# Performance work log

Measured on AMD Instinct MI355X. Metric: run time of the kernel, lower is better.

The kernel has to match this reference:

```python
import jax, jax.numpy as jnp
import numpy as np

D_MODEL = 1024
N_HEAD = 16
D_K = D_MODEL // N_HEAD


def setup_inputs() -> dict:
    key = jax.random.key(0)
    ks = jax.random.split(key, 11)
    B, T = 2, 2048
    s = 1.0 / np.sqrt(D_MODEL)
    return {
        "q": jax.random.normal(ks[0], (B, T, D_MODEL), jnp.float32),
        "k": jax.random.normal(ks[1], (B, T, D_MODEL), jnp.float32),
        "v": jax.random.normal(ks[2], (B, T, D_MODEL), jnp.float32),
        "w_q": jax.random.normal(ks[3], (D_MODEL, D_MODEL), jnp.float32) * s,
        "b_q": jax.random.normal(ks[4], (D_MODEL,), jnp.float32) * 0.01,
        "w_k": jax.random.normal(ks[5], (D_MODEL, D_MODEL), jnp.float32) * s,
        "b_k": jax.random.normal(ks[6], (D_MODEL,), jnp.float32) * 0.01,
        "w_v": jax.random.normal(ks[7], (D_MODEL, D_MODEL), jnp.float32) * s,
        "b_v": jax.random.normal(ks[8], (D_MODEL,), jnp.float32) * 0.01,
        "w_o": jax.random.normal(ks[9], (D_MODEL, D_MODEL), jnp.float32) * s,
        "b_o": jax.random.normal(ks[10], (D_MODEL,), jnp.float32) * 0.01,
    }


def reference(q, k, v, w_q, b_q, w_k, b_k, w_v, b_v, w_o, b_o):
    B, T, _ = q.shape
    # QKV projections -> [B, H, T, d_k]
    def proj(x, w, b):
        return (jnp.einsum('btd,de->bte', x, w) + b).reshape(B, T, N_HEAD, D_K).transpose(0, 2, 1, 3)
    qh = proj(q, w_q, b_q)
    kh = proj(k, w_k, b_k)
    vh = proj(v, w_v, b_v)
    scale = jnp.float32(1.0 / np.sqrt(D_K))
    scores = jnp.einsum('bhqd,bhkd->bhqk', qh, kh) * scale  # [B,H,T,T]
    attn = jax.nn.softmax(scores, axis=-1)
    # dropout is identity in eval mode
    out = jnp.einsum('bhqk,bhkd->bhqd', attn, vh)  # [B,H,T,d_k]
    out = out.transpose(0, 2, 1, 3).reshape(B, T, N_HEAD * D_K)
    return jnp.einsum('btd,de->bte', out, w_o) + b_o
```

## Files before the change

### kernel.cpp

```cpp
#include <hip/hip_runtime.h>
#include <stdint.h>

#define DEVI static __device__ __forceinline__

typedef float f32x4 __attribute__((ext_vector_type(4)));
typedef float f32x16 __attribute__((ext_vector_type(16)));
typedef short s16x8 __attribute__((ext_vector_type(8)));
typedef unsigned short u16x4 __attribute__((ext_vector_type(4)));
typedef uint32_t u32x2 __attribute__((ext_vector_type(2)));
typedef uint32_t u32x4 __attribute__((ext_vector_type(4)));

DEVI unsigned short f2bf(float f) {
  union { float f; uint32_t u; } v; v.f = f;
  uint32_t u = v.u;
  return (unsigned short)((u + 0x7fffu + ((u >> 16) & 1u)) >> 16);
}

DEVI float bf2f(unsigned short u) {
  union { uint32_t u; float f; } v;
  v.u = ((uint32_t)u) << 16;
  return v.f;
}

DEVI uint32_t cvtpk(float lo, float hi) {
  uint32_t r;
  asm("v_cvt_pk_bf16_f32 %0, %1, %2" : "=v"(r) : "v"(lo), "v"(hi));
  return r;
}

DEVI float fexp2(float x) {
#if __has_builtin(__builtin_amdgcn_exp2f)
  return __builtin_amdgcn_exp2f(x);
#else
  return exp2f(x);
#endif
}

DEVI void pl32swap(uint32_t& a, uint32_t& b) {
#if __has_builtin(__builtin_amdgcn_permlane32_swap)
  u32x2 r = __builtin_amdgcn_permlane32_swap(a, b, false, false);
  a = r[0]; b = r[1];
#else
  asm("v_permlane32_swap_b32 %0, %1" : "+v"(a), "+v"(b));
#endif
}

DEVI float swap_half(float x, int hi) {
  uint32_t a = __float_as_uint(x), b = a;
  pl32swap(a, b);
  return hi ? __uint_as_float(a) : __uint_as_float(b);
}

DEVI void g2l16(const void* g, void* l) {
  __builtin_amdgcn_global_load_lds(
      (const __attribute__((address_space(1))) void*)g,
      (__attribute__((address_space(3))) void*)l, 16, 0, 0);
}

DEVI float vmax16(const f32x16& v) {
  float a = fmaxf(fmaxf(v[0], v[1]), fmaxf(v[2], v[3]));
  float b = fmaxf(fmaxf(v[4], v[5]), fmaxf(v[6], v[7]));
  float c = fmaxf(fmaxf(v[8], v[9]), fmaxf(v[10], v[11]));
  float d = fmaxf(fmaxf(v[12], v[13]), fmaxf(v[14], v[15]));
  return fmaxf(fmaxf(a, b), fmaxf(c, d));
}

DEVI float vsum16(const f32x16& v) {
  float a = (v[0] + v[1]) + (v[2] + v[3]);
  float b = (v[4] + v[5]) + (v[6] + v[7]);
  float c = (v[8] + v[9]) + (v[10] + v[11]);
  float d = (v[12] + v[13]) + (v[14] + v[15]);
  return (a + b) + (c + d);
}

__global__ __launch_bounds__(256) void k_cvt3(const float* __restrict__ q,
                                              const float* __restrict__ k,
                                              const float* __restrict__ v,
                                              unsigned short* __restrict__ out) {
  const int y = blockIdx.y;
  const float* in = y == 0 ? q : y == 1 ? k : v;
  unsigned short* o = out + (size_t)y * 4194304;
  int idx = blockIdx.x * blockDim.x + threadIdx.x;
  int stride = gridDim.x * blockDim.x;
  for (int i = idx * 4; i < 4194304; i += stride * 4) {
    f32x4 x = *(const f32x4*)(in + i);
    u16x4 r;
    for (int j = 0; j < 4; ++j) r[j] = f2bf(x[j]);
    *(u16x4*)(o + i) = r;
  }
}

__global__ __launch_bounds__(256) void k_wt4(const float* w0, const float* w1,
                                             const float* w2, const float* w3,
                                             unsigned short* t0, unsigned short* t1,
                                             unsigned short* t2, unsigned short* t3) {
  const int z = blockIdx.z;
  const float* w = z == 0 ? w0 : z == 1 ? w1 : z == 2 ? w2 : w3;
  unsigned short* wt = z == 0 ? t0 : z == 1 ? t1 : z == 2 ? t2 : t3;
  __shared__ float tile[32][33];
  const int tx = threadIdx.x, ty = threadIdx.y;
  const int n0 = blockIdx.x * 32, k0 = blockIdx.y * 32;
  for (int j = 0; j < 4; ++j)
    tile[ty + j * 8][tx] = w[(size_t)(k0 + ty + j * 8) * 1024 + n0 + tx];
  __syncthreads();
  for (int j = 0; j < 4; ++j)
    wt[(size_t)(n0 + ty + j * 8) * 1024 + k0 + tx] = f2bf(tile[tx][ty + j * 8]);
}

__global__ __launch_bounds__(256) void k_gemm_multi(
    const unsigned short* A0, const unsigned short* A1, const unsigned short* A2,
    const unsigned short* B0, const unsigned short* B1, const unsigned short* B2,
    const float* c0, const float* c1, const float* c2,
    void* o0, void* o1, void* o2, int mode0) {
  constexpr int K = 1024;
  const int z = blockIdx.y;
  const unsigned short* A = z == 0 ? A0 : z == 1 ? A1 : A2;
  const unsigned short* Bt = z == 0 ? B0 : z == 1 ? B1 : B2;
  const float* bias = z == 0 ? c0 : z == 1 ? c1 : c2;
  void* outp = z == 0 ? o0 : z == 1 ? o1 : o2;
  const int MODE = mode0 + z;

  __shared__ __align__(16) unsigned short As[128 * 64];
  __shared__ __align__(16) unsigned short Bs[64 * 64];
  const int tid = threadIdx.x;
  const int lane = tid & 63, w = tid >> 6;
  const int g = lane >> 4, c = lane & 15;
  const int wgid = (blockIdx.x & 7) * 64 + (blockIdx.x >> 3);
  const int bm = wgid >> 4, bn = wgid & 15;
  const int m0 = bm * 128, n0 = bn * 64;
  const int wr = w >> 1, wc = w & 1;
  f32x4 acc[4][2] = {};

  for (int kt = 0; kt < 16; ++kt) {
    const int k0 = kt * 64;
    __syncthreads();
#pragma unroll
    for (int it = 0; it < 4; ++it) {
      int e = it * 256 + tid;
      int row = e >> 3, cwp = (e & 7) ^ (row & 7);
      g2l16(A + (size_t)(m0 + row) * K + k0 + cwp * 8,
            (char*)As + (it * 256 + (w << 6)) * 16);
    }
#pragma unroll
    for (int it = 0; it < 2; ++it) {
      int e = it * 256 + tid;
      int row = e >> 3, cwp = (e & 7) ^ (row & 7);
      g2l16(Bt + (size_t)(n0 + row) * K + k0 + cwp * 8,
            (char*)Bs + (it * 256 + (w << 6)) * 16);
    }
    __syncthreads();
    for (int kk = 0; kk < 2; ++kk) {
      s16x8 af[4], bfr[2];
      for (int mi = 0; mi < 4; ++mi) {
        int row = wr * 64 + mi * 16 + c;
        int ch = (kk * 4 + g) ^ (row & 7);
        af[mi] = *(const s16x8*)((const char*)As + row * 128 + ch * 16);
      }
      for (int ni = 0; ni < 2; ++ni) {
        int row = wc * 32 + ni * 16 + c;
        int ch = (kk * 4 + g) ^ (row & 7);
        bfr[ni] = *(const s16x8*)((const char*)Bs + row * 128 + ch * 16);
      }
      for (int mi = 0; mi < 4; ++mi)
        for (int ni = 0; ni < 2; ++ni)
          acc[mi][ni] = __builtin_amdgcn_mfma_f32_16x16x32_bf16(
              af[mi], bfr[ni], acc[mi][ni], 0, 0, 0);
    }
  }

  if (MODE == 0 || MODE == 1) {
    unsigned short* out = (unsigned short*)outp;
    const float scale = (MODE == 0) ? 0.1803368801111204f : 1.0f;
    for (int mi = 0; mi < 4; ++mi)
      for (int ni = 0; ni < 2; ++ni) {
        int row = m0 + wr * 64 + mi * 16 + g * 4;
        int col = n0 + wc * 32 + ni * 16 + c;
        float bb = bias[col];
        for (int r = 0; r < 4; ++r)
          out[(size_t)(row + r) * 1024 + col] = f2bf((acc[mi][ni][r] + bb) * scale);
      }
  } else if (MODE == 2) {
    unsigned short* vt = (unsigned short*)outp;
    const int bq = m0 >> 11, t0 = m0 & 2047;
    for (int mi = 0; mi < 4; ++mi)
      for (int ni = 0; ni < 2; ++ni) {
        int rowb = wr * 64 + mi * 16 + g * 4;
        int coll = wc * 32 + ni * 16 + c;
        float bb = bias[n0 + coll];
        u16x4 pk;
        for (int r = 0; r < 4; ++r) pk[r] = f2bf(acc[mi][ni][r] + bb);
        *(u16x4*)(vt + (size_t)(bq * 1024 + n0 + coll) * 2048 + t0 + rowb) = pk;
      }
  } else {
    float* out = (float*)outp;
    for (int mi = 0; mi < 4; ++mi)
      for (int ni = 0; ni < 2; ++ni) {
        int row = m0 + wr * 64 + mi * 16 + g * 4;
        int col = n0 + wc * 32 + ni * 16 + c;
        float bb = bias[col];
        for (int r = 0; r < 4; ++r)
          out[(size_t)(row + r) * 1024 + col] = acc[mi][ni][r] + bb;
      }
  }
}

__global__ __launch_bounds__(256) void k_attn(const unsigned short* __restrict__ Qp,
                                              const unsigned short* __restrict__ Kp,
                                              const unsigned short* __restrict__ Vt,
                                              unsigned short* __restrict__ Po0,
                                              unsigned short* __restrict__ Po1,
                                              float2* __restrict__ ml) {
  __shared__ __align__(16) unsigned short Ks[2][4096];
  __shared__ __align__(16) unsigned short Vs[2][4096];
  const int tid = threadIdx.x;
  const int lane = tid & 63, w = tid >> 6;
  const int l31 = lane & 31, hi = lane >> 5;
  const int blk = (blockIdx.x & 7) * 128 + (blockIdx.x >> 3);
  const int half = blk & 1, qt = (blk >> 1) & 15, bh = blk >> 5;
  const int b = bh >> 4, h = bh & 15;
  const int m0 = qt * 128 + w * 32;
  const size_t qkBase = (size_t)b * 2048 * 1024 + (size_t)h * 64;
  const size_t vtBase = ((size_t)b * 1024 + h * 64) * 2048;

  const unsigned short* qrow = Qp + qkBase + (size_t)(m0 + l31) * 1024;
  s16x8 bq[4];
#pragma unroll
  for (int s = 0; s < 4; ++s)
    bq[s] = *(const s16x8*)(qrow + s * 16 + hi * 8);

  const int srow = tid >> 2, c4 = tid & 3;
  const unsigned short* kg = Kp + qkBase + (size_t)srow * 1024 + c4 * 16 +
                             (size_t)half * 1048576;
  const unsigned short* vg = Vt + vtBase + (size_t)srow * 2048 + c4 * 16 +
                             half * 1024;
  int wof[2];
#pragma unroll
  for (int j = 0; j < 2; ++j)
    wof[j] = srow * 128 + (((c4 * 2 + j) ^ (srow & 7)) * 16);

  float m_run = -1e30f, l_run = 0.f;
  f32x16 o0 = {}, o1 = {};

  {
    s16x8 k0 = *(const s16x8*)(kg), k1 = *(const s16x8*)(kg + 8);
    s16x8 v0 = *(const s16x8*)(vg), v1 = *(const s16x8*)(vg + 8);
    *(s16x8*)((char*)&Ks[0][0] + wof[0]) = k0;
    *(s16x8*)((char*)&Ks[0][0] + wof[1]) = k1;
    *(s16x8*)((char*)&Vs[0][0] + wof[0]) = v0;
    *(s16x8*)((char*)&Vs[0][0] + wof[1]) = v1;
  }
  __syncthreads();

  const int rch = l31 & 7;

#pragma unroll 1
  for (int t = 0; t < 16; ++t) {
    const int cur = t & 1;
    s16x8 k0, k1, v0, v1;
    if (t < 15) {
      const unsigned short* kgt = kg + (size_t)(t + 1) * 65536;
      const unsigned short* vgt = vg + (t + 1) * 64;
      k0 = *(const s16x8*)(kgt); k1 = *(const s16x8*)(kgt + 8);
      v0 = *(const s16x8*)(vgt); v1 = *(const s16x8*)(vgt + 8);
    }
    const char* ks = (const char*)&Ks[cur][0];
    const char* vs = (const char*)&Vs[cur][0];

    f32x16 s0 = {}, s1 = {};
    __builtin_amdgcn_s_setprio(1);
#pragma unroll
    for (int ds = 0; ds < 4; ++ds) {
      int ch = (2 * ds + hi) ^ rch;
      s16x8 a0 = *(const s16x8*)(ks + l31 * 128 + ch * 16);
      s16x8 a1 = *(const s16x8*)(ks + (32 + l31) * 128 + ch * 16);
      s0 = __builtin_amdgcn_mfma_f32_32x32x16_bf16(a0, bq[ds], s0, 0, 0, 0);
      s1 = __builtin_amdgcn_mfma_f32_32x32x16_bf16(a1, bq[ds], s1, 0, 0, 0);
    }
    __builtin_amdgcn_s_setprio(0);

    float tm = fmaxf(vmax16(s0), vmax16(s1));
    tm = fmaxf(tm, swap_half(tm, hi));
    if (!__all(tm - m_run <= 8.0f)) {
      float mt = fmaxf(m_run, tm);
      float al = fexp2(m_run - mt);
      l_run *= al;
#pragma unroll
      for (int j = 0; j < 16; ++j) { o0[j] *= al; o1[j] *= al; }
      m_run = mt;
    }
#pragma unroll
    for (int j = 0; j < 16; ++j) s0[j] = fexp2(s0[j] - m_run);
#pragma unroll
    for (int j = 0; j < 16; ++j) s1[j] = fexp2(s1[j] - m_run);
    l_run += vsum16(s0) + vsum16(s1);

    s16x8 pf[4];
    {
      uint32_t w0 = cvtpk(s0[0], s0[1]), w1 = cvtpk(s0[2], s0[3]);
      uint32_t w2 = cvtpk(s0[4], s0[5]), w3 = cvtpk(s0[6], s0[7]);
      uint32_t w4 = cvtpk(s0[8], s0[9]), w5 = cvtpk(s0[10], s0[11]);
      uint32_t w6 = cvtpk(s0[12], s0[13]), w7 = cvtpk(s0[14], s0[15]);
      pl32swap(w0, w2); pl32swap(w1, w3); pl32swap(w4, w6); pl32swap(w5, w7);
      u32x4 f0 = {w0, w1, w2, w3}, f1 = {w4, w5, w6, w7};
      pf[0] = *(s16x8*)&f0;
      pf[1] = *(s16x8*)&f1;
    }
    {
      uint32_t w0 = cvtpk(s1[0], s1[1]), w1 = cvtpk(s1[2], s1[3]);
      uint32_t w2 = cvtpk(s1[4], s1[5]), w3 = cvtpk(s1[6], s1[7]);
      uint32_t w4 = cvtpk(s1[8], s1[9]), w5 = cvtpk(s1[10], s1[11]);
      uint32_t w6 = cvtpk(s1[12], s1[13]), w7 = cvtpk(s1[14], s1[15]);
      pl32swap(w0, w2); pl32swap(w1, w3); pl32swap(w4, w6); pl32swap(w5, w7);
      u32x4 f0 = {w0, w1, w2, w3}, f1 = {w4, w5, w6, w7};
      pf[2] = *(s16x8*)&f0;
      pf[3] = *(s16x8*)&f1;
    }

    __builtin_amdgcn_s_setprio(1);
#pragma unroll
    for (int ksp = 0; ksp < 4; ++ksp) {
      int ch = (2 * ksp + hi) ^ rch;
      s16x8 a0 = *(const s16x8*)(vs + l31 * 128 + ch * 16);
      s16x8 a1 = *(const s16x8*)(vs + (32 + l31) * 128 + ch * 16);
      o0 = __builtin_amdgcn_mfma_f32_32x32x16_bf16(a0, pf[ksp], o0, 0, 0, 0);
      o1 = __builtin_amdgcn_mfma_f32_32x32x16_bf16(a1, pf[ksp], o1, 0, 0, 0);
    }
    __builtin_amdgcn_s_setprio(0);

    if (t < 15) {
      const int nb = cur ^ 1;
      *(s16x8*)((char*)&Ks[nb][0] + wof[0]) = k0;
      *(s16x8*)((char*)&Ks[nb][0] + wof[1]) = k1;
      *(s16x8*)((char*)&Vs[nb][0] + wof[0]) = v0;
      *(s16x8*)((char*)&Vs[nb][0] + wof[1]) = v1;
    }
    __syncthreads();
  }

  float lt = l_run + swap_half(l_run, hi);
  float inv = 1.0f / lt;
  unsigned short* Po = half ? Po1 : Po0;
  unsigned short* arow = Po + ((size_t)b * 2048 + m0 + l31) * 1024 + h * 64;
#pragma unroll
  for (int dblk = 0; dblk < 2; ++dblk) {
#pragma unroll
    for (int rq = 0; rq < 4; ++rq) {
      float e0 = (dblk ? o1[rq * 4 + 0] : o0[rq * 4 + 0]) * inv;
      float e1 = (dblk ? o1[rq * 4 + 1] : o0[rq * 4 + 1]) * inv;
      float e2 = (dblk ? o1[rq * 4 + 2] : o0[rq * 4 + 2]) * inv;
      float e3 = (dblk ? o1[rq * 4 + 3] : o0[rq * 4 + 3]) * inv;
      u32x2 pk;
      pk[0] = cvtpk(e0, e1);
      pk[1] = cvtpk(e2, e3);
      *(u32x2*)(arow + dblk * 32 + 8 * rq + 4 * hi) = pk;
    }
  }
  if (hi == 0) {
    int qid = ((b << 4) + h) * 2048 + m0 + l31;
    ml[half * 65536 + qid] = {m_run, lt};
  }
}

__global__ __launch_bounds__(256) void k_comb(const unsigned short* __restrict__ Po0,
                                              const unsigned short* __restrict__ Po1,
                                              const float2* __restrict__ ml,
                                              unsigned short* __restrict__ Att) {
  int idx = blockIdx.x * 256 + threadIdx.x;
  int base = idx * 8;
  int qrow = base >> 10, col = base & 1023;
  int h = col >> 6, b = qrow >> 11, t = qrow & 2047;
  int qid = ((b << 4) + h) * 2048 + t;
  float2 p0 = ml[qid], p1 = ml[65536 + qid];
  float ms = fmaxf(p0.x, p1.x);
  float a0 = fexp2(p0.x - ms) * p0.y, a1 = fexp2(p1.x - ms) * p1.y;
  float inv = 1.0f / (a0 + a1);
  float w0 = a0 * inv, w1 = a1 * inv;
  s16x8 v0 = *(const s16x8*)(Po0 + base);
  s16x8 v1 = *(const s16x8*)(Po1 + base);
  u32x4 pk;
#pragma unroll
  for (int j = 0; j < 4; ++j) {
    float e0 = w0 * bf2f((unsigned short)v0[2 * j]) + w1 * bf2f((unsigned short)v1[2 * j]);
    float e1 = w0 * bf2f((unsigned short)v0[2 * j + 1]) + w1 * bf2f((unsigned short)v1[2 * j + 1]);
    pk[j] = cvtpk(e0, e1);
  }
  *(u32x4*)(Att + base) = pk;
}

extern "C" void kernel_launch(void* const* d_in, const int* in_sizes, int n_in,
                              void* d_out, int out_size, void* d_ws, size_t ws_size,
                              hipStream_t stream) {
  const float* q = (const float*)d_in[0];
  const float* k = (const float*)d_in[1];
  const float* v = (const float*)d_in[2];
  const float* w_q = (const float*)d_in[3];
  const float* b_q = (const float*)d_in[4];
  const float* w_k = (const float*)d_in[5];
  const float* b_k = (const float*)d_in[6];
  const float* w_v = (const float*)d_in[7];
  const float* b_v = (const float*)d_in[8];
  const float* w_o = (const float*)d_in[9];
  const float* b_o = (const float*)d_in[10];

  unsigned short* s = (unsigned short*)d_ws;
  unsigned short* qbf = s;
  unsigned short* kbf = s + 4194304;
  unsigned short* vbf = s + 8388608;
  unsigned short* wqT = s + 12582912;
  unsigned short* wkT = s + 13631488;
  unsigned short* wvT = s + 14680064;
  unsigned short* woT = s + 15728640;
  unsigned short* Qp  = s + 16777216;
  unsigned short* Kp  = s + 20971520;
  unsigned short* Vt  = s + 25165824;
  unsigned short* Po0 = qbf;
  unsigned short* Po1 = kbf;
  unsigned short* Att = vbf;
  float2* ml = (float2*)wqT;

  k_cvt3<<<dim3(1024, 3), 256, 0, stream>>>(q, k, v, qbf);

  k_wt4<<<dim3(32, 32, 4), dim3(32, 8), 0, stream>>>(w_q, w_k, w_v, w_o,
                                                     wqT, wkT, wvT, woT);

  k_gemm_multi<<<dim3(512, 3), 256, 0, stream>>>(
      qbf, kbf, vbf, wqT, wkT, wvT, b_q, b_k, b_v,
      (void*)Qp, (void*)Kp, (void*)Vt, 0);

  k_attn<<<1024, 256, 0, stream>>>(Qp, Kp, Vt, Po0, Po1, ml);

  k_comb<<<2048, 256, 0, stream>>>(Po0, Po1, ml, Att);

  k_gemm_multi<<<dim3(512, 1), 256, 0, stream>>>(
      Att, Att, Att, woT, woT, woT, b_o, b_o, b_o,
      d_out, d_out, d_out, 3);
}
```

Baseline: 134.7 us.

## Async LDS staging in attention, MFMA row sums, max3, merged prep kernel

The attention kernel now stages K/V tiles straight into LDS with global_load_lds instead of going through registers and writing to LDS after the compute, so the next tile's copy overlaps the current compute. The softmax row sum is computed by an extra MFMA against a vector of ones rather than VALU reductions. The max reduction uses v_max3, and the input conversion and weight transpose kernels are merged into a single launch. These add MFMA work and change the swizzle and loading layout. The swizzle stays consistent only if the per-wave LDS offsets match the prior layout.

Result: no change. 136.9 us (+1.6%).

```diff
diff --git a/kernel.cpp b/kernel.cpp
--- a/kernel.cpp
+++ b/kernel.cpp
@@ -34,6 +34,12 @@
 #else
   return exp2f(x);
 #endif
+}
+
+DEVI float max3(float a, float b, float c) {
+  float r;
+  asm("v_max3_f32 %0, %1, %2, %3" : "=v"(r) : "v"(a), "v"(b), "v"(c));
+  return r;
 }
 
 DEVI void pl32swap(uint32_t& a, uint32_t& b) {
@@ -58,53 +64,49 @@
 }
 
 DEVI float vmax16(const f32x16& v) {
-  float a = fmaxf(fmaxf(v[0], v[1]), fmaxf(v[2], v[3]));
-  float b = fmaxf(fmaxf(v[4], v[5]), fmaxf(v[6], v[7]));
-  float c = fmaxf(fmaxf(v[8], v[9]), fmaxf(v[10], v[11]));
-  float d = fmaxf(fmaxf(v[12], v[13]), fmaxf(v[14], v[15]));
-  return fmaxf(fmaxf(a, b), fmaxf(c, d));
-}
-
-DEVI float vsum16(const f32x16& v) {
-  float a = (v[0] + v[1]) + (v[2] + v[3]);
-  float b = (v[4] + v[5]) + (v[6] + v[7]);
-  float c = (v[8] + v[9]) + (v[10] + v[11]);
-  float d = (v[12] + v[13]) + (v[14] + v[15]);
-  return (a + b) + (c + d);
-}
-
-__global__ __launch_bounds__(256) void k_cvt3(const float* __restrict__ q,
-                                              const float* __restrict__ k,
-                                              const float* __restrict__ v,
-                                              unsigned short* __restrict__ out) {
-  const int y = blockIdx.y;
-  const float* in = y == 0 ? q : y == 1 ? k : v;
-  unsigned short* o = out + (size_t)y * 4194304;
-  int idx = blockIdx.x * blockDim.x + threadIdx.x;
-  int stride = gridDim.x * blockDim.x;
-  for (int i = idx * 4; i < 4194304; i += stride * 4) {
-    f32x4 x = *(const f32x4*)(in + i);
-    u16x4 r;
-    for (int j = 0; j < 4; ++j) r[j] = f2bf(x[j]);
-    *(u16x4*)(o + i) = r;
-  }
-}
-
-__global__ __launch_bounds__(256) void k_wt4(const float* w0, const float* w1,
-                                             const float* w2, const float* w3,
-                                             unsigned short* t0, unsigned short* t1,
-                                             unsigned short* t2, unsigned short* t3) {
-  const int z = blockIdx.z;
-  const float* w = z == 0 ? w0 : z == 1 ? w1 : z == 2 ? w2 : w3;
-  unsigned short* wt = z == 0 ? t0 : z == 1 ? t1 : z == 2 ? t2 : t3;
+  float a = max3(v[0], v[1], v[2]);
+  float b = max3(v[3], v[4], v[5]);
+  float c = max3(v[6], v[7], v[8]);
+  float d = max3(v[9], v[10], v[11]);
+  float e = max3(v[12], v[13], v[14]);
+  float x = max3(a, b, c);
+  float y = max3(d, e, v[15]);
+  return fmaxf(x, y);
+}
+
+__global__ __launch_bounds__(256) void k_prep(
+    const float* __restrict__ q, const float* __restrict__ k,
+    const float* __restrict__ v, unsigned short* __restrict__ qkv,
+    const float* __restrict__ w0, const float* __restrict__ w1,
+    const float* __restrict__ w2, const float* __restrict__ w3,
+    unsigned short* __restrict__ t0, unsigned short* __restrict__ t1,
+    unsigned short* __restrict__ t2, unsigned short* __restrict__ t3) {
   __shared__ float tile[32][33];
-  const int tx = threadIdx.x, ty = threadIdx.y;
-  const int n0 = blockIdx.x * 32, k0 = blockIdx.y * 32;
-  for (int j = 0; j < 4; ++j)
-    tile[ty + j * 8][tx] = w[(size_t)(k0 + ty + j * 8) * 1024 + n0 + tx];
-  __syncthreads();
-  for (int j = 0; j < 4; ++j)
-    wt[(size_t)(n0 + ty + j * 8) * 1024 + k0 + tx] = f2bf(tile[tx][ty + j * 8]);
+  const int bx = blockIdx.x;
+  if (bx < 3072) {
+    const int y = bx >> 10;
+    const float* in = y == 0 ? q : y == 1 ? k : v;
+    unsigned short* o = qkv + (size_t)y * 4194304;
+    int idx = (bx & 1023) * 256 + threadIdx.x;
+    for (int i = idx * 4; i < 4194304; i += 1048576) {
+      f32x4 x = *(const f32x4*)(in + i);
+      u16x4 r;
+      for (int j = 0; j < 4; ++j) r[j] = f2bf(x[j]);
+      *(u16x4*)(o + i) = r;
+    }
+  } else {
+    const int wb = bx - 3072;
+    const int z = wb >> 10, tb = wb & 1023;
+    const float* w = z == 0 ? w0 : z == 1 ? w1 : z == 2 ? w2 : w3;
+    unsigned short* wt = z == 0 ? t0 : z == 1 ? t1 : z == 2 ? t2 : t3;
+    const int n0 = (tb & 31) * 32, k0 = (tb >> 5) * 32;
+    const int tx = threadIdx.x & 31, ty = threadIdx.x >> 5;
+    for (int j = 0; j < 4; ++j)
+      tile[ty + j * 8][tx] = w[(size_t)(k0 + ty + j * 8) * 1024 + n0 + tx];
+    __syncthreads();
+    for (int j = 0; j < 4; ++j)
+      wt[(size_t)(n0 + ty + j * 8) * 1024 + k0 + tx] = f2bf(tile[tx][ty + j * 8]);
+  }
 }
 
 __global__ __launch_bounds__(256) void k_gemm_multi(
@@ -228,27 +230,30 @@
   for (int s = 0; s < 4; ++s)
     bq[s] = *(const s16x8*)(qrow + s * 16 + hi * 8);
 
-  const int srow = tid >> 2, c4 = tid & 3;
-  const unsigned short* kg = Kp + qkBase + (size_t)srow * 1024 + c4 * 16 +
-                             (size_t)half * 1048576;
-  const unsigned short* vg = Vt + vtBase + (size_t)srow * 2048 + c4 * 16 +
-                             half * 1024;
-  int wof[2];
-#pragma unroll
-  for (int j = 0; j < 2; ++j)
-    wof[j] = srow * 128 + (((c4 * 2 + j) ^ (srow & 7)) * 16);
-
-  float m_run = -1e30f, l_run = 0.f;
-  f32x16 o0 = {}, o1 = {};
-
-  {
-    s16x8 k0 = *(const s16x8*)(kg), k1 = *(const s16x8*)(kg + 8);
-    s16x8 v0 = *(const s16x8*)(vg), v1 = *(const s16x8*)(vg + 8);
-    *(s16x8*)((char*)&Ks[0][0] + wof[0]) = k0;
-    *(s16x8*)((char*)&Ks[0][0] + wof[1]) = k1;
-    *(s16x8*)((char*)&Vs[0][0] + wof[0]) = v0;
-    *(s16x8*)((char*)&Vs[0][0] + wof[1]) = v1;
-  }
+  const int r0 = tid >> 3, c0 = tid & 7;
+  const int csw = (c0 ^ (r0 & 7)) * 8;
+  const unsigned short* ks0 = Kp + qkBase + (size_t)half * 1048576 +
+                              (size_t)r0 * 1024 + csw;
+  const unsigned short* vs0 = Vt + vtBase + (size_t)r0 * 2048 + half * 1024 + csw;
+  const int ldw = w * 1024;
+
+  auto stage = [&](int buf, int t) {
+    const size_t ko = (size_t)t * 65536;
+    const int vo = t * 64;
+    char* kb = (char*)&Ks[buf][0];
+    char* vb = (char*)&Vs[buf][0];
+    g2l16(ks0 + ko, kb + ldw);
+    g2l16(ks0 + ko + 32 * 1024, kb + 4096 + ldw);
+    g2l16(vs0 + vo, vb + ldw);
+    g2l16(vs0 + vo + 32 * 2048, vb + 4096 + ldw);
+  };
+
+  float m_run = -1e30f;
+  f32x16 o0 = {}, o1 = {}, la = {};
+  const u32x4 onev = {0x3F803F80u, 0x3F803F80u, 0x3F803F80u, 0x3F803F80u};
+  const s16x8 ones = *(const s16x8*)&onev;
+
+  stage(0, 0);
   __syncthreads();
 
   const int rch = l31 & 7;
@@ -256,13 +261,7 @@
 #pragma unroll 1
   for (int t = 0; t < 16; ++t) {
     const int cur = t & 1;
-    s16x8 k0, k1, v0, v1;
-    if (t < 15) {
-      const unsigned short* kgt = kg + (size_t)(t + 1) * 65536;
-      const unsigned short* vgt = vg + (t + 1) * 64;
-      k0 = *(const s16x8*)(kgt); k1 = *(const s16x8*)(kgt + 8);
-      v0 = *(const s16x8*)(vgt); v1 = *(const s16x8*)(vgt + 8);
-    }
+    if (t < 15) stage(cur ^ 1, t + 1);
     const char* ks = (const char*)&Ks[cur][0];
     const char* vs = (const char*)&Vs[cur][0];
 
@@ -283,7 +282,7 @@
     if (!__all(tm - m_run <= 8.0f)) {
       float mt = fmaxf(m_run, tm);
       float al = fexp2(m_run - mt);
-      l_run *= al;
+      la[0] *= al;
 #pragma unroll
       for (int j = 0; j < 16; ++j) { o0[j] *= al; o1[j] *= al; }
       m_run = mt;
@@ -292,7 +291,6 @@
     for (int j = 0; j < 16; ++j) s0[j] = fexp2(s0[j] - m_run);
 #pragma unroll
     for (int j = 0; j < 16; ++j) s1[j] = fexp2(s1[j] - m_run);
-    l_run += vsum16(s0) + vsum16(s1);
 
     s16x8 pf[4];
     {
@@ -324,20 +322,14 @@
       s16x8 a1 = *(const s16x8*)(vs + (32 + l31) * 128 + ch * 16);
       o0 = __builtin_amdgcn_mfma_f32_32x32x16_bf16(a0, pf[ksp], o0, 0, 0, 0);
       o1 = __builtin_amdgcn_mfma_f32_32x32x16_bf16(a1, pf[ksp], o1, 0, 0, 0);
+      la = __builtin_amdgcn_mfma_f32_32x32x16_bf16(ones, pf[ksp], la, 0, 0, 0);
     }
     __builtin_amdgcn_s_setprio(0);
 
-    if (t < 15) {
-      const int nb = cur ^ 1;
-      *(s16x8*)((char*)&Ks[nb][0] + wof[0]) = k0;
-      *(s16x8*)((char*)&Ks[nb][0] + wof[1]) = k1;
-      *(s16x8*)((char*)&Vs[nb][0] + wof[0]) = v0;
-      *(s16x8*)((char*)&Vs[nb][0] + wof[1]) = v1;
-    }
     __syncthreads();
   }
 
-  float lt = l_run + swap_half(l_run, hi);
+  float lt = la[0];
   float inv = 1.0f / lt;
   unsigned short* Po = half ? Po1 : Po0;
   unsigned short* arow = Po + ((size_t)b * 2048 + m0 + l31) * 1024 + h * 64;
@@ -418,10 +410,8 @@
   unsigned short* Att = vbf;
   float2* ml = (float2*)wqT;
 
-  k_cvt3<<<dim3(1024, 3), 256, 0, stream>>>(q, k, v, qbf);
-
-  k_wt4<<<dim3(32, 32, 4), dim3(32, 8), 0, stream>>>(w_q, w_k, w_v, w_o,
-                                                     wqT, wkT, wvT, woT);
+  k_prep<<<7168, 256, 0, stream>>>(q, k, v, qbf, w_q, w_k, w_v, w_o,
+                                   wqT, wkT, wvT, woT);
 
   k_gemm_multi<<<dim3(512, 3), 256, 0, stream>>>(
       qbf, kbf, vbf, wqT, wkT, wvT, b_q, b_k, b_v,
```
